# Kernel optimization log

Hardware: AMD Instinct MI355X
Metric: run time of the kernel (lower is better)

Reference implementation:

```python
import math
import jax, jax.numpy as jnp
from jax import lax
import numpy as np

B, SEQ, D_MODEL = 8, 1024, 512
R, K, H = 3, 3, 4
DE, DH, DU, DTR, DCONV, DEMB = 64, 64, 32, 4, 3, 10


def setup_inputs() -> dict:
    key = jax.random.key(0)
    ks = iter(jax.random.split(key, 48))
    def nrm(shape, s=0.05):
        return jax.random.normal(next(ks), shape, jnp.float32) * s
    inp = {}
    inp['x'] = jax.random.normal(next(ks), (B, SEQ, D_MODEL), jnp.float32)
    # Mamba params, leading dims (R, 2) = (layer, fwd/bwd direction)
    inp['m_in_w'] = nrm((R, 2, D_MODEL, 2 * DE))
    inp['m_conv_w'] = nrm((R, 2, DE, DCONV), 0.2)
    inp['m_conv_b'] = nrm((R, 2, DE), 0.1)
    inp['m_xproj_w'] = nrm((R, 2, DE, DTR + 2 * DH))
    inp['m_dt_w'] = nrm((R, 2, DTR, DE), 0.2)
    inp['m_dt_b'] = nrm((R, 2, DE), 0.1)
    inp['m_Alog'] = jnp.broadcast_to(jnp.log(jnp.arange(1, DH + 1, dtype=jnp.float32)), (R, 2, DE, DH)) + jnp.zeros((R, 2, DE, DH), jnp.float32)
    inp['m_D'] = jnp.ones((R, 2, DE), jnp.float32)
    inp['m_out_w'] = nrm((R, 2, DE, D_MODEL))
    # LayerNorm / FFN params per layer
    inp['ln1_g'] = jnp.ones((R, D_MODEL), jnp.float32)
    inp['ln1_b'] = jnp.zeros((R, D_MODEL), jnp.float32)
    inp['ffn_w1'] = nrm((R, D_MODEL, DU))
    inp['ffn_b1'] = jnp.zeros((R, DU), jnp.float32)
    inp['ffn_w2'] = nrm((R, DU, D_MODEL))
    inp['ffn_b2'] = jnp.zeros((R, D_MODEL), jnp.float32)
    inp['ln2_g'] = jnp.ones((R, D_MODEL), jnp.float32)
    inp['ln2_b'] = jnp.zeros((R, D_MODEL), jnp.float32)
    # MAGAC params (N = D_MODEL nodes, in_dim = SEQ)
    inp['psi_emb'] = jax.random.normal(next(ks), (D_MODEL, DEMB), jnp.float32)
    inp['psi'] = jnp.array(1.0, jnp.float32)
    inp['W_q'] = jax.random.normal(next(ks), (DEMB, H, DEMB), jnp.float32)
    inp['W_k'] = jax.random.normal(next(ks), (DEMB, H, DEMB), jnp.float32)
    inp['attn_alpha'] = jnp.array(0.5, jnp.float32)
    inp['F_w'] = nrm((H, DEMB, K + 1, SEQ))
    inp['f_b'] = jax.random.normal(next(ks), (H, DEMB), jnp.float32)
    inp['head_mix'] = jnp.ones((H,), jnp.float32)
    inp['head_w'] = nrm((D_MODEL,))
    inp['head_b'] = jnp.zeros((), jnp.float32)
    return inp


def _layernorm(x, g, b, eps=1e-5):
    mu = x.mean(-1, keepdims=True)
    v = ((x - mu) ** 2).mean(-1, keepdims=True)
    return (x - mu) / jnp.sqrt(v + eps) * g + b


def _mamba(x, in_w, conv_w, conv_b, xproj_w, dt_w, dt_b, Alog, Dp, out_w):
    b, l, _ = x.shape
    xr = x @ in_w                              # (b,l,2*DE)
    xp, res = jnp.split(xr, 2, axis=-1)
    # depthwise causal conv (torch pads k-1 both sides then truncates to l == left-pad k-1)
    xc = xp.transpose(0, 2, 1)                 # (b,DE,l)
    xc = lax.conv_general_dilated(xc, conv_w[:, None, :], (1,), [(DCONV - 1, 0)],
                                  feature_group_count=DE,
                                  dimension_numbers=('NCH', 'OIH', 'NCH'))
    xc = xc + conv_b[None, :, None]
    xp = jax.nn.silu(xc.transpose(0, 2, 1))    # (b,l,DE)
    A = -jnp.exp(Alog)                         # (DE,DH)
    x_dbl = xp @ xproj_w                       # (b,l,DTR+2*DH)
    delta = jax.nn.softplus(x_dbl[..., :DTR] @ dt_w + dt_b)   # (b,l,DE)
    Bm = x_dbl[..., DTR:DTR + DH]
    Cm = x_dbl[..., DTR + DH:]
    dA = jnp.exp(delta[..., None] * A)                         # (b,l,DE,DH)
    dBu = delta[..., None] * Bm[:, :, None, :] * xp[..., None] # (b,l,DE,DH)
    def step(s, inp):
        dAt, dBt, ct = inp
        s = dAt * s + dBt
        return s, jnp.einsum('bdn,bn->bd', s, ct)
    s0 = jnp.zeros((b, DE, DH), x.dtype)
    _, ys = lax.scan(step, s0, (dA.transpose(1, 0, 2, 3), dBu.transpose(1, 0, 2, 3), Cm.transpose(1, 0, 2)))
    y = ys.transpose(1, 0, 2) + xp * Dp
    y = y * jax.nn.sigmoid(res)
    return y @ out_w


def _magac(xg, psi_emb, psi, W_q, W_k, attn_alpha, F_w, f_b, head_mix):
    # xg: (B, N, L); eval-mode deterministic path
    diff = psi_emb[:, None, :] - psi_emb[None, :, :]
    A_base = jax.nn.softmax(jnp.exp(-psi * (diff ** 2).sum(-1)), axis=1)   # (N,N)
    Q = jnp.einsum('nd,dhm->nhm', psi_emb, W_q)
    Kq = jnp.einsum('nd,dhm->nhm', psi_emb, W_k)
    attn = jax.nn.softmax(jnp.einsum('nhd,mhd->hnm', Q, Kq) / math.sqrt(DEMB), axis=-1)
    alpha = jax.nn.sigmoid(attn_alpha)
    A_eff = alpha * A_base[None] + (1.0 - alpha) * attn                    # (H,N,N)
    N = psi_emb.shape[0]
    I = jnp.broadcast_to(jnp.eye(N, dtype=xg.dtype), (H, N, N))
    sup = [I, A_eff]
    for _ in range(K - 1):
        sup.append(2.0 * jnp.matmul(A_eff, sup[-1]) - sup[-2])             # Chebyshev
    sup = jnp.stack(sup, axis=1)                                           # (H,K+1,N,N)
    Wf = jnp.einsum('nd,hdkl->hnkl', psi_emb, F_w)                         # (H,N,K+1,L)
    bf = jnp.einsum('nd,hd->hn', psi_emb, f_b)                             # (H,N)
    x_g = jnp.einsum('hknm,bml->bhknl', sup, xg)                           # (B,H,K+1,N,L)
    out_h = jnp.einsum('bhknl,hnkl->bhn', x_g, Wf) + bf[None]
    mix = jax.nn.softmax(head_mix)
    return jnp.einsum('bhn,h->bn', out_h, mix)


def reference(x, m_in_w, m_conv_w, m_conv_b, m_xproj_w, m_dt_w, m_dt_b, m_Alog, m_D, m_out_w,
              ln1_g, ln1_b, ffn_w1, ffn_b1, ffn_w2, ffn_b2, ln2_g, ln2_b,
              psi_emb, psi, W_q, W_k, attn_alpha, F_w, f_b, head_mix, head_w, head_b):
    for i in range(R):
        mf = (m_in_w[i, 0], m_conv_w[i, 0], m_conv_b[i, 0], m_xproj_w[i, 0], m_dt_w[i, 0],
              m_dt_b[i, 0], m_Alog[i, 0], m_D[i, 0], m_out_w[i, 0])
        mb = (m_in_w[i, 1], m_conv_w[i, 1], m_conv_b[i, 1], m_xproj_w[i, 1], m_dt_w[i, 1],
              m_dt_b[i, 1], m_Alog[i, 1], m_D[i, 1], m_out_w[i, 1])
        y_f = _mamba(x, *mf)
        y_b = jnp.flip(_mamba(jnp.flip(x, 1), *mb), 1)
        y = _layernorm(x + y_f + y_b, ln1_g[i], ln1_b[i])
        z = jax.nn.relu(y @ ffn_w1[i] + ffn_b1[i]) @ ffn_w2[i] + ffn_b2[i]
        x = _layernorm(y + z, ln2_g[i], ln2_b[i])
    g = _magac(x.transpose(0, 2, 1), psi_emb, psi, W_q, W_k, attn_alpha, F_w, f_b, head_mix)
    # eval-mode Bayesian MC: all mc_eval samples identical -> mean=g, var=1e-6
    log_var_node = jnp.full_like(g, jnp.log(jnp.asarray(1e-6, g.dtype)))
    mu = g @ head_w + head_b
    var = jnp.exp(log_var_node) @ (head_w ** 2) + 1e-6
    return mu, jnp.log(var)
```

## Files before the change

### kernel.cpp

```cpp
#include <hip/hip_runtime.h>
#include <math.h>

#define SEQL 1024
#define NB 8
#define DMOD 512

__device__ __forceinline__ float blk_sum4(float v, volatile float* sb) {
#pragma unroll
  for (int off = 32; off; off >>= 1) v += __shfl_xor(v, off, 64);
  int lid = threadIdx.x & 63, wid = threadIdx.x >> 6;
  if (lid == 0) sb[wid] = v;
  __syncthreads();
  float t = sb[0] + sb[1] + sb[2] + sb[3];
  __syncthreads();
  return t;
}
__device__ __forceinline__ float blk_max4(float v, volatile float* sb) {
#pragma unroll
  for (int off = 32; off; off >>= 1) v = fmaxf(v, __shfl_xor(v, off, 64));
  int lid = threadIdx.x & 63, wid = threadIdx.x >> 6;
  if (lid == 0) sb[wid] = v;
  __syncthreads();
  float t = fmaxf(fmaxf(sb[0], sb[1]), fmaxf(sb[2], sb[3]));
  __syncthreads();
  return t;
}

__global__ __launch_bounds__(256) void gemm_f32(
    const float* __restrict__ A, long aStr,
    const float* __restrict__ B, long bStr,
    const float* __restrict__ Dm, long dStr,
    float* __restrict__ C, long cStr, long cChunkStr,
    int M, int N, int K, int lda, int ldb, int ldd, int ldc,
    float alpha, float beta, int kchunks) {
  __shared__ float As[16][68];
  __shared__ float Bs[16][64];
  const int zz = blockIdx.z;
  const int zb = zz / kchunks, kc = zz % kchunks;
  A += (long)zb * aStr + (long)kc * K;
  B += (long)zb * bStr + (long)kc * K * ldb;
  Dm += (long)zb * dStr;
  C += (long)zb * cStr + (long)kc * cChunkStr;
  const int tid = threadIdx.x;
  const int m0 = blockIdx.y * 64, n0 = blockIdx.x * 64;
  const int tx = tid & 15, ty = tid >> 4;
  const int arow = tid >> 2, acol = (tid & 3) << 2;
  const int brow = tid >> 4, bcol = (tid & 15) << 2;
  const bool aOk = (m0 + arow < M);
  const float* Aptr = A + (long)(m0 + arow) * lda + acol;
  const float* Bptr = B + (long)brow * ldb;
  const int bc = n0 + bcol;
  const int kIters = K >> 4;
  float acc[4][4] = {};

  auto loadB = [&](int it) {
    const float* Bk = Bptr + (long)it * 16 * ldb;
    float4 r;
    if (bc + 3 < N) r = *(const float4*)(Bk + bc);
    else {
      r.x = (bc + 0 < N) ? Bk[bc + 0] : 0.f;
      r.y = (bc + 1 < N) ? Bk[bc + 1] : 0.f;
      r.z = (bc + 2 < N) ? Bk[bc + 2] : 0.f;
      r.w = (bc + 3 < N) ? Bk[bc + 3] : 0.f;
    }
    return r;
  };

  float4 av = make_float4(0.f, 0.f, 0.f, 0.f);
  if (aOk) av = *(const float4*)(Aptr);
  float4 bv = loadB(0);

  for (int it = 0; it < kIters; ++it) {
    As[acol + 0][arow] = av.x; As[acol + 1][arow] = av.y;
    As[acol + 2][arow] = av.z; As[acol + 3][arow] = av.w;
    *(float4*)&Bs[brow][bcol] = bv;
    __syncthreads();
    if (it + 1 < kIters) {
      if (aOk) av = *(const float4*)(Aptr + (it + 1) * 16);
      bv = loadB(it + 1);
    }
#pragma unroll
    for (int kk = 0; kk < 16; ++kk) {
      float4 aq = *(const float4*)&As[kk][ty << 2];
      float4 bq = *(const float4*)&Bs[kk][tx << 2];
      float aa[4] = {aq.x, aq.y, aq.z, aq.w};
      float bb[4] = {bq.x, bq.y, bq.z, bq.w};
#pragma unroll
      for (int i = 0; i < 4; ++i)
#pragma unroll
        for (int j = 0; j < 4; ++j) acc[i][j] = fmaf(aa[i], bb[j], acc[i][j]);
    }
    __syncthreads();
  }
#pragma unroll
  for (int i = 0; i < 4; ++i) {
    int row = m0 + (ty << 2) + i;
    if (row >= M) continue;
#pragma unroll
    for (int j = 0; j < 4; ++j) {
      int col = n0 + (tx << 2) + j;
      if (col >= N) continue;
      float v = alpha * acc[i][j];
      if (beta != 0.f) v += beta * Dm[(long)row * ldd + col];
      C[(long)row * ldc + col] = v;
    }
  }
}

__global__ __launch_bounds__(256) void conv_silu(
    const float* __restrict__ xr, float* __restrict__ xp,
    const float* __restrict__ cw, const float* __restrict__ cb) {
  int dir = blockIdx.y;
  int idx = blockIdx.x * 256 + threadIdx.x;
  const float* xrp = xr + (long)dir * 1048576;
  float* xpp = xp + (long)dir * 524288;
  const float* w = cw + dir * 192;
  int e = idx & 63;
  int t = (idx >> 6) & 1023;
  long rb = (long)(idx >> 6) * 128;
  float w0 = w[e * 3 + 0], w1 = w[e * 3 + 1], w2 = w[e * 3 + 2];
  float acc = cb[dir * 64 + e] + w2 * xrp[rb + e];
  if (dir == 0) {
    if (t >= 1) acc += w1 * xrp[rb - 128 + e];
    if (t >= 2) acc += w0 * xrp[rb - 256 + e];
  } else {
    if (t <= 1022) acc += w1 * xrp[rb + 128 + e];
    if (t <= 1021) acc += w0 * xrp[rb + 256 + e];
  }
  xpp[idx] = acc / (1.f + __expf(-acc));
}

__global__ __launch_bounds__(64) void proj_kernel(
    const float* __restrict__ xp, const float* __restrict__ pw,
    const float* __restrict__ dw, const float* __restrict__ db,
    float* __restrict__ dl, float* __restrict__ Bm, float* __restrict__ Cm) {
  int tok = blockIdx.x, dir = blockIdx.y, j = threadIdx.x;
  const float* xpp = xp + (long)dir * 524288 + (long)tok * 64;
  const float* w = pw + dir * 8448;
  __shared__ float xs[64];
  __shared__ float dpre[4];
  xs[j] = xpp[j];
  __syncthreads();
  float aB = 0.f, aC = 0.f, aD = 0.f;
  for (int k = 0; k < 64; ++k) {
    float xv = xs[k];
    const float* wr = w + k * 132;
    aB = fmaf(xv, wr[4 + j], aB);
    aC = fmaf(xv, wr[68 + j], aC);
    aD = fmaf(xv, wr[j & 3], aD);
  }
  long ob = (long)dir * 524288 + (long)tok * 64;
  Bm[ob + j] = aB;
  Cm[ob + j] = aC;
  if (j < 4) dpre[j] = aD;
  __syncthreads();
  const float* dwp = dw + dir * 256;
  float dv = db[dir * 64 + j];
#pragma unroll
  for (int r = 0; r < 4; ++r) dv = fmaf(dpre[r], dwp[r * 64 + j], dv);
  dl[ob + j] = fmaxf(dv, 0.f) + log1pf(__expf(-fabsf(dv)));
}

__global__ __launch_bounds__(64) void scan_p1(
    const float* __restrict__ dl, const float* __restrict__ Bm,
    const float* __restrict__ xp, const float* __restrict__ Alog,
    float* __restrict__ Aprod, float* __restrict__ Send) {
  int d = blockIdx.x, b = blockIdx.y;
  int dir = blockIdx.z >> 4, c = blockIdx.z & 15;
  int n = threadIdx.x;
  long doff = (long)dir * 524288;
  int tln = c * 64 + n;
  int tgn = dir ? 1023 - tln : tln;
  float dlv_v = dl[doff + ((long)b * 1024 + tgn) * 64 + d];
  float xpv_v = xp[doff + ((long)b * 1024 + tgn) * 64 + d];
  float a_dn = -__expf(Alog[dir * 4096 + d * 64 + n]);
  const float* Bp = Bm + doff + (long)b * 65536;
  float s = 0.f, ap = 1.f;
#pragma unroll 8
  for (int st = 0; st < 64; ++st) {
    float dlv = __shfl(dlv_v, st);
    float xpv = __shfl(xpv_v, st);
    int tl = c * 64 + st;
    int tg = dir ? 1023 - tl : tl;
    float bt = Bp[(long)tg * 64 + n];
    float a = __expf(dlv * a_dn);
    ap *= a;
    s = fmaf(a, s, (dlv * xpv) * bt);
  }
  long sidx = ((long)((dir * 8 + b) * 64 + d)) * 1024 + c * 64 + n;
  Aprod[sidx] = ap;
  Send[sidx] = s;
}

__global__ __launch_bounds__(64) void scan_p2(
    const float* __restrict__ Aprod, const float* __restrict__ Send,
    float* __restrict__ Sin) {
  int d = blockIdx.x, b = blockIdx.y, dir = blockIdx.z;
  int n = threadIdx.x;
  long base = ((long)((dir * 8 + b) * 64 + d)) * 1024;
  float s = 0.f;
#pragma unroll
  for (int c = 0; c < 16; ++c) {
    Sin[base + c * 64 + n] = s;
    s = fmaf(Aprod[base + c * 64 + n], s, Send[base + c * 64 + n]);
  }
}

__global__ __launch_bounds__(64) void scan_p3(
    const float* __restrict__ dl, const float* __restrict__ Bm,
    const float* __restrict__ Cm, const float* __restrict__ xp,
    const float* __restrict__ xr, const float* __restrict__ Alog,
    const float* __restrict__ Dp, const float* __restrict__ Sin,
    float* __restrict__ ycat) {
  __shared__ float sP[16 * 65];
  int d = blockIdx.x, b = blockIdx.y;
  int dir = blockIdx.z >> 4, c = blockIdx.z & 15;
  int n = threadIdx.x;
  long doff = (long)dir * 524288;
  int tln = c * 64 + n;
  int tgn = dir ? 1023 - tln : tln;
  float dlv_v = dl[doff + ((long)b * 1024 + tgn) * 64 + d];
  float xpv_v = xp[doff + ((long)b * 1024 + tgn) * 64 + d];
  float a_dn = -__expf(Alog[dir * 4096 + d * 64 + n]);
  float dpd = Dp[dir * 64 + d];
  const float* Bp = Bm + doff + (long)b * 65536;
  const float* Cp = Cm + doff + (long)b * 65536;
  const float* xrp = xr + (long)dir * 1048576 + (long)b * 131072;
  long sidx = ((long)((dir * 8 + b) * 64 + d)) * 1024 + c * 64 + n;
  float s = Sin[sidx];
  int r4 = n >> 2, q4 = n & 3;
  for (int sb = 0; sb < 4; ++sb) {
#pragma unroll
    for (int k = 0; k < 16; ++k) {
      int st = sb * 16 + k;
      float dlv = __shfl(dlv_v, st);
      float xpv = __shfl(xpv_v, st);
      int tl = c * 64 + st;
      int tg = dir ? 1023 - tl : tl;
      float bt = Bp[(long)tg * 64 + n];
      float ct = Cp[(long)tg * 64 + n];
      float a = __expf(dlv * a_dn);
      s = fmaf(a, s, (dlv * xpv) * bt);
      sP[k * 65 + n] = s * ct;
    }
    __syncthreads();
    float p = 0.f;
#pragma unroll
    for (int k = 0; k < 16; ++k) p += sP[r4 * 65 + q4 * 16 + k];
    p += __shfl_xor(p, 1, 64);
    p += __shfl_xor(p, 2, 64);
    float xpv_r = __shfl(xpv_v, sb * 16 + r4);
    if (q4 == 0) {
      int tl = c * 64 + sb * 16 + r4;
      int tg = dir ? 1023 - tl : tl;
      float rres = xrp[(long)tg * 128 + 64 + d];
      ycat[((long)b * 1024 + tg) * 128 + dir * 64 + d] =
          (p + xpv_r * dpd) * (1.f / (1.f + __expf(-rres)));
    }
    __syncthreads();
  }
}

__global__ __launch_bounds__(256) void ln_ffn_ln(
    float* __restrict__ x, const float* __restrict__ g1, const float* __restrict__ b1v,
    const float* __restrict__ w1, const float* __restrict__ bb1,
    const float* __restrict__ w2, const float* __restrict__ bb2,
    const float* __restrict__ g2, const float* __restrict__ b2v) {
  __shared__ float ybuf[512];
  __shared__ float rbuf[256];
  __shared__ float zbuf[32];
  __shared__ float red[4];
  int tok = blockIdx.x, tid = threadIdx.x;
  float* row = x + (long)tok * 512;
  float v0 = row[tid], v1 = row[tid + 256];
  float mu = blk_sum4(v0 + v1, red) * (1.f / 512.f);
  float d0 = v0 - mu, d1 = v1 - mu;
  float var = blk_sum4(d0 * d0 + d1 * d1, red) * (1.f / 512.f);
  float rstd = 1.f / sqrtf(var + 1e-5f);
  float y0 = d0 * rstd * g1[tid] + b1v[tid];
  float y1 = d1 * rstd * g1[tid + 256] + b1v[tid + 256];
  ybuf[tid] = y0; ybuf[tid + 256] = y1;
  __syncthreads();
  int u = tid & 31, seg = tid >> 5;
  float p = 0.f;
  int k0 = seg * 64;
#pragma unroll 8
  for (int k = 0; k < 64; ++k) p = fmaf(ybuf[k0 + k], w1[(k0 + k) * 32 + u], p);
  rbuf[seg * 32 + u] = p;
  __syncthreads();
  if (tid < 32) {
    float zv = bb1[tid];
#pragma unroll
    for (int sg = 0; sg < 8; ++sg) zv += rbuf[sg * 32 + tid];
    zbuf[tid] = fmaxf(zv, 0.f);
  }
  __syncthreads();
  float h0 = y0 + bb2[tid];
  float h1 = y1 + bb2[tid + 256];
#pragma unroll
  for (int uu = 0; uu < 32; ++uu) {
    float zv = zbuf[uu];
    h0 = fmaf(zv, w2[uu * 512 + tid], h0);
    h1 = fmaf(zv, w2[uu * 512 + tid + 256], h1);
  }
  float mu2 = blk_sum4(h0 + h1, red) * (1.f / 512.f);
  float e0 = h0 - mu2, e1 = h1 - mu2;
  float var2 = blk_sum4(e0 * e0 + e1 * e1, red) * (1.f / 512.f);
  float rstd2 = 1.f / sqrtf(var2 + 1e-5f);
  row[tid] = e0 * rstd2 * g2[tid] + b2v[tid];
  row[tid + 256] = e1 * rstd2 * g2[tid + 256] + b2v[tid + 256];
}

__global__ __launch_bounds__(64) void qk_kernel(
    const float* __restrict__ e, const float* __restrict__ Wq,
    const float* __restrict__ Wk, float* __restrict__ Qb, float* __restrict__ Kb) {
  int n = blockIdx.x, j = threadIdx.x;
  __shared__ float en[10];
  if (j < 10) en[j] = e[n * 10 + j];
  __syncthreads();
  if (j < 40) {
    float q = 0.f, k = 0.f;
#pragma unroll
    for (int dd = 0; dd < 10; ++dd) {
      q = fmaf(en[dd], Wq[dd * 40 + j], q);
      k = fmaf(en[dd], Wk[dd * 40 + j], k);
    }
    Qb[n * 40 + j] = q;
    Kb[n * 40 + j] = k;
  }
}

__global__ __launch_bounds__(256) void aeff_kernel(
    const float* __restrict__ e, const float* __restrict__ Qb,
    const float* __restrict__ Kb, const float* __restrict__ psi_p,
    const float* __restrict__ alpha_p, float* __restrict__ Aef) {
  int n = blockIdx.x, h = blockIdx.y, tid = threadIdx.x;
  __shared__ float s_at[512];
  __shared__ float s_bs[512];
  __shared__ float qn[10];
  __shared__ float en[10];
  __shared__ float red[4];
  if (tid < 10) { qn[tid] = Qb[n * 40 + h * 10 + tid]; en[tid] = e[n * 10 + tid]; }
  __syncthreads();
  float psi = psi_p[0];
  float alpha = 1.f / (1.f + __expf(-alpha_p[0]));
  const float isq = 0.3162277660168379f;
  for (int m = tid; m < 512; m += 256) {
    float sc = 0.f, d2 = 0.f;
#pragma unroll
    for (int dd = 0; dd < 10; ++dd) {
      sc = fmaf(qn[dd], Kb[m * 40 + h * 10 + dd], sc);
      float df = en[dd] - e[m * 10 + dd];
      d2 = fmaf(df, df, d2);
    }
    s_at[m] = sc * isq;
    s_bs[m] = __expf(-psi * d2);
  }
  __syncthreads();
  float m1 = -1e30f, m2 = -1e30f;
  for (int m = tid; m < 512; m += 256) { m1 = fmaxf(m1, s_at[m]); m2 = fmaxf(m2, s_bs[m]); }
  m1 = blk_max4(m1, red);
  m2 = blk_max4(m2, red);
  float e1 = 0.f, e2 = 0.f;
  for (int m = tid; m < 512; m += 256) {
    float a = __expf(s_at[m] - m1); s_at[m] = a; e1 += a;
    float bq = __expf(s_bs[m] - m2); s_bs[m] = bq; e2 += bq;
  }
  e1 = blk_sum4(e1, red);
  e2 = blk_sum4(e2, red);
  float r1 = (1.f - alpha) / e1, r2 = alpha / e2;
  float* outp = Aef + (long)h * 262144 + (long)n * 512;
  for (int m = tid; m < 512; m += 256) outp[m] = r2 * s_bs[m] + r1 * s_at[m];
}

__global__ void xpose_kernel(const float* __restrict__ DbufP,
                             float* __restrict__ X3, float* __restrict__ X2s,
                             float* __restrict__ X13, float* __restrict__ X02) {
  int idx = blockIdx.x * 256 + threadIdx.x;
  if (idx >= 163840) return;
  int c = idx % 80;
  int m = (idx / 80) % 512;
  int h = idx / 40960;
  int d = c >> 3, b = c & 7;
  long base = (long)(b * 160 + h * 40 + d * 4) * 512 + m;
  float k0 = 0.f, k1 = 0.f, k2 = 0.f, k3 = 0.f;
#pragma unroll
  for (int p = 0; p < 4; ++p) {
    const float* Dp_ = DbufP + (long)p * 655360;
    k0 += Dp_[base];
    k1 += Dp_[base + 512];
    k2 += Dp_[base + 1024];
    k3 += Dp_[base + 1536];
  }
  X3[idx] = k3;
  X2s[idx] = k2;
  X13[idx] = k1 - 3.f * k3;
  X02[idx] = k0 - k2;
}

__global__ void outh_kernel(const float* __restrict__ e, const float* __restrict__ fb,
                            const float* __restrict__ Zt, const float* __restrict__ hm,
                            float* __restrict__ g) {
  int idx = blockIdx.x * 256 + threadIdx.x;
  if (idx >= 4096) return;
  int n = idx & 511, b = idx >> 9;
  float h0 = hm[0], h1 = hm[1], h2 = hm[2], h3 = hm[3];
  float mx = fmaxf(fmaxf(h0, h1), fmaxf(h2, h3));
  float x0 = __expf(h0 - mx), x1 = __expf(h1 - mx), x2 = __expf(h2 - mx), x3 = __expf(h3 - mx);
  float es = x0 + x1 + x2 + x3;
  float mixv[4] = {x0 / es, x1 / es, x2 / es, x3 / es};
  float acc = 0.f;
  for (int h = 0; h < 4; ++h) {
    float oh = 0.f;
#pragma unroll
    for (int dd = 0; dd < 10; ++dd) {
      float ev = e[n * 10 + dd];
      float v = Zt[((long)h * 512 + n) * 80 + dd * 8 + b] + fb[h * 10 + dd];
      oh = fmaf(ev, v, oh);
    }
    acc = fmaf(mixv[h], oh, acc);
  }
  g[b * 512 + n] = acc;
}

__global__ __launch_bounds__(256) void head_kernel(
    const float* __restrict__ g, const float* __restrict__ hw,
    const float* __restrict__ hb, float* __restrict__ out) {
  __shared__ float red[4];
  int b = blockIdx.x, tid = threadIdx.x;
  float w0 = hw[tid], w1 = hw[tid + 256];
  float v = g[b * 512 + tid] * w0 + g[b * 512 + tid + 256] * w1;
  float q = w0 * w0 + w1 * w1;
  float mu = blk_sum4(v, red);
  float s2 = blk_sum4(q, red);
  if (tid == 0) {
    out[b] = mu + hb[0];
    out[8 + b] = logf(1e-6f * s2 + 1e-6f);
  }
}

extern "C" void kernel_launch(void* const* d_in, const int* in_sizes, int n_in,
                              void* d_out, int out_size, void* d_ws, size_t ws_size,
                              hipStream_t stream) {
  (void)in_sizes; (void)n_in; (void)out_size; (void)ws_size;
  const float* x0    = (const float*)d_in[0];
  const float* in_w  = (const float*)d_in[1];
  const float* cw    = (const float*)d_in[2];
  const float* cb    = (const float*)d_in[3];
  const float* pw    = (const float*)d_in[4];
  const float* dtw   = (const float*)d_in[5];
  const float* dtb   = (const float*)d_in[6];
  const float* Alog  = (const float*)d_in[7];
  const float* Dpar  = (const float*)d_in[8];
  const float* ow    = (const float*)d_in[9];
  const float* l1g   = (const float*)d_in[10];
  const float* l1b   = (const float*)d_in[11];
  const float* fw1   = (const float*)d_in[12];
  const float* fb1   = (const float*)d_in[13];
  const float* fw2   = (const float*)d_in[14];
  const float* fb2   = (const float*)d_in[15];
  const float* l2g   = (const float*)d_in[16];
  const float* l2b   = (const float*)d_in[17];
  const float* emb   = (const float*)d_in[18];
  const float* psi   = (const float*)d_in[19];
  const float* Wq    = (const float*)d_in[20];
  const float* Wk    = (const float*)d_in[21];
  const float* aal   = (const float*)d_in[22];
  const float* Fw    = (const float*)d_in[23];
  const float* fbv   = (const float*)d_in[24];
  const float* hmix  = (const float*)d_in[25];
  const float* hw    = (const float*)d_in[26];
  const float* hb    = (const float*)d_in[27];
  float* out = (float*)d_out;

  float* ws = (float*)d_ws;
  float* xA   = ws;
  float* xB   = xA + 4194304;
  float* scr  = xB + 4194304;
  float* xr   = scr;
  float* xp   = xr + 2097152;
  float* dl   = xp + 1048576;
  float* Bm   = dl + 1048576;
  float* Cm   = Bm + 1048576;
  float* ycat = Cm + 1048576;
  float* Aprod = scr + 7340032;
  float* Send  = Aprod + 1048576;
  float* Sin   = Send + 1048576;
  float* Qb    = scr;
  float* Kb    = Qb + 20480;
  float* Aef   = Kb + 20480;
  float* DbufP = Aef + 1048576;
  float* X3    = DbufP + 2621440;
  float* X2s   = X3 + 163840;
  float* X13   = X2s + 163840;
  float* X02   = X13 + 163840;
  float* Z2    = X02 + 163840;
  float* Z1    = Z2 + 163840;
  float* Zt    = Z1 + 163840;
  float* gb    = Zt + 163840;

  const float* xin = x0;
  float* bufs[3] = {xA, xB, xA};
  for (int i = 0; i < 3; ++i) {
    float* xout = bufs[i];
    gemm_f32<<<dim3(2, 128, 2), 256, 0, stream>>>(
        xin, 0, in_w + (long)i * 131072, 65536, xin, 0, xr, 1048576, 0,
        8192, 128, 512, 512, 128, 0, 128, 1.f, 0.f, 1);
    conv_silu<<<dim3(2048, 2), 256, 0, stream>>>(xr, xp, cw + i * 384, cb + i * 128);
    proj_kernel<<<dim3(8192, 2), 64, 0, stream>>>(
        xp, pw + i * 16896, dtw + i * 512, dtb + i * 128, dl, Bm, Cm);
    scan_p1<<<dim3(64, 8, 32), 64, 0, stream>>>(
        dl, Bm, xp, Alog + i * 8192, Aprod, Send);
    scan_p2<<<dim3(64, 8, 2), 64, 0, stream>>>(Aprod, Send, Sin);
    scan_p3<<<dim3(64, 8, 32), 64, 0, stream>>>(
        dl, Bm, Cm, xp, xr, Alog + i * 8192, Dpar + i * 128, Sin, ycat);
    gemm_f32<<<dim3(8, 128, 1), 256, 0, stream>>>(
        ycat, 0, ow + (long)i * 65536, 0, xin, 0, xout, 0, 0,
        8192, 512, 128, 128, 512, 512, 512, 1.f, 1.f, 1);
    ln_ffn_ln<<<8192, 256, 0, stream>>>(
        xout, l1g + i * 512, l1b + i * 512, fw1 + i * 16384, fb1 + i * 32,
        fw2 + i * 16384, fb2 + i * 512, l2g + i * 512, l2b + i * 512);
    xin = xout;
  }
  qk_kernel<<<512, 64, 0, stream>>>(emb, Wq, Wk, Qb, Kb);
  aeff_kernel<<<dim3(512, 4), 256, 0, stream>>>(emb, Qb, Kb, psi, aal, Aef);
  gemm_f32<<<dim3(8, 3, 32), 256, 0, stream>>>(
      Fw, 0, xA, 524288, Fw, 0, DbufP, 81920, 655360,
      160, 512, 256, 1024, 512, 0, 512, 1.f, 0.f, 4);
  xpose_kernel<<<640, 256, 0, stream>>>(DbufP, X3, X2s, X13, X02);
  gemm_f32<<<dim3(2, 8, 4), 256, 0, stream>>>(
      Aef, 262144, X3, 40960, X2s, 40960, Z2, 40960, 0,
      512, 80, 512, 512, 80, 80, 80, 4.f, 2.f, 1);
  gemm_f32<<<dim3(2, 8, 4), 256, 0, stream>>>(
      Aef, 262144, Z2, 40960, X13, 40960, Z1, 40960, 0,
      512, 80, 512, 512, 80, 80, 80, 1.f, 1.f, 1);
  gemm_f32<<<dim3(2, 8, 4), 256, 0, stream>>>(
      Aef, 262144, Z1, 40960, X02, 40960, Zt, 40960, 0,
      512, 80, 512, 512, 80, 80, 80, 1.f, 1.f, 1);
  outh_kernel<<<16, 256, 0, stream>>>(emb, fbv, Zt, hmix, gb);
  head_kernel<<<8, 256, 0, stream>>>(gb, hw, hb, out);
}
```

Before: 825.9 us.

## Double-buffer GEMM shared tiles and process two tokens per LN-FFN block

The GEMM kernel now uses ping-pong shared-memory buffers for its A and B tiles. This drops one barrier per k-iteration and lets the store of the next tile follow the compute on the current one. The fused LayerNorm-FFN-LayerNorm kernel now handles two tokens per block, reusing each w1/w2 weight load across both tokens. It also computes mean and variance in a single pass (sum and sum of squares), which removes two of the block reductions. The single-pass variance is slightly less numerically robust, and the doubled shared memory may lower occupancy.

```diff
diff --git a/kernel.cpp b/kernel.cpp
--- a/kernel.cpp
+++ b/kernel.cpp
@@ -33,8 +33,8 @@
     float* __restrict__ C, long cStr, long cChunkStr,
     int M, int N, int K, int lda, int ldb, int ldd, int ldc,
     float alpha, float beta, int kchunks) {
-  __shared__ float As[16][68];
-  __shared__ float Bs[16][64];
+  __shared__ float As[2][16][68];
+  __shared__ float Bs[2][16][64];
   const int zz = blockIdx.z;
   const int zb = zz / kchunks, kc = zz % kchunks;
   A += (long)zb * aStr + (long)kc * K;
@@ -69,20 +69,22 @@
   float4 av = make_float4(0.f, 0.f, 0.f, 0.f);
   if (aOk) av = *(const float4*)(Aptr);
   float4 bv = loadB(0);
+  As[0][acol + 0][arow] = av.x; As[0][acol + 1][arow] = av.y;
+  As[0][acol + 2][arow] = av.z; As[0][acol + 3][arow] = av.w;
+  *(float4*)&Bs[0][brow][bcol] = bv;
 
   for (int it = 0; it < kIters; ++it) {
-    As[acol + 0][arow] = av.x; As[acol + 1][arow] = av.y;
-    As[acol + 2][arow] = av.z; As[acol + 3][arow] = av.w;
-    *(float4*)&Bs[brow][bcol] = bv;
+    const int cur = it & 1;
     __syncthreads();
-    if (it + 1 < kIters) {
+    const bool more = (it + 1 < kIters);
+    if (more) {
       if (aOk) av = *(const float4*)(Aptr + (it + 1) * 16);
       bv = loadB(it + 1);
     }
 #pragma unroll
     for (int kk = 0; kk < 16; ++kk) {
-      float4 aq = *(const float4*)&As[kk][ty << 2];
-      float4 bq = *(const float4*)&Bs[kk][tx << 2];
+      float4 aq = *(const float4*)&As[cur][kk][ty << 2];
+      float4 bq = *(const float4*)&Bs[cur][kk][tx << 2];
       float aa[4] = {aq.x, aq.y, aq.z, aq.w};
       float bb[4] = {bq.x, bq.y, bq.z, bq.w};
 #pragma unroll
@@ -90,7 +92,12 @@
 #pragma unroll
         for (int j = 0; j < 4; ++j) acc[i][j] = fmaf(aa[i], bb[j], acc[i][j]);
     }
-    __syncthreads();
+    if (more) {
+      const int nxt = cur ^ 1;
+      As[nxt][acol + 0][arow] = av.x; As[nxt][acol + 1][arow] = av.y;
+      As[nxt][acol + 2][arow] = av.z; As[nxt][acol + 3][arow] = av.w;
+      *(float4*)&Bs[nxt][brow][bcol] = bv;
+    }
   }
 #pragma unroll
   for (int i = 0; i < 4; ++i) {
@@ -266,49 +273,105 @@
     const float* __restrict__ w1, const float* __restrict__ bb1,
     const float* __restrict__ w2, const float* __restrict__ bb2,
     const float* __restrict__ g2, const float* __restrict__ b2v) {
-  __shared__ float ybuf[512];
-  __shared__ float rbuf[256];
-  __shared__ float zbuf[32];
-  __shared__ float red[4];
-  int tok = blockIdx.x, tid = threadIdx.x;
-  float* row = x + (long)tok * 512;
-  float v0 = row[tid], v1 = row[tid + 256];
-  float mu = blk_sum4(v0 + v1, red) * (1.f / 512.f);
-  float d0 = v0 - mu, d1 = v1 - mu;
-  float var = blk_sum4(d0 * d0 + d1 * d1, red) * (1.f / 512.f);
-  float rstd = 1.f / sqrtf(var + 1e-5f);
-  float y0 = d0 * rstd * g1[tid] + b1v[tid];
-  float y1 = d1 * rstd * g1[tid + 256] + b1v[tid + 256];
-  ybuf[tid] = y0; ybuf[tid + 256] = y1;
+  __shared__ float ybuf[2][512];
+  __shared__ float rbuf[2][256];
+  __shared__ float zbuf[2][32];
+  __shared__ float red4[16];
+  int tid = threadIdx.x;
+  int lid = tid & 63, wid = tid >> 6;
+  float* row0 = x + (long)blockIdx.x * 1024;
+  float* row1 = row0 + 512;
+  float a0 = row0[tid], b0 = row0[tid + 256];
+  float a1 = row1[tid], b1 = row1[tid + 256];
+  float s0 = a0 + b0, q0 = a0 * a0 + b0 * b0;
+  float s1 = a1 + b1, q1 = a1 * a1 + b1 * b1;
+#pragma unroll
+  for (int off = 32; off; off >>= 1) {
+    s0 += __shfl_xor(s0, off, 64); q0 += __shfl_xor(q0, off, 64);
+    s1 += __shfl_xor(s1, off, 64); q1 += __shfl_xor(q1, off, 64);
+  }
+  if (lid == 0) {
+    red4[wid * 4 + 0] = s0; red4[wid * 4 + 1] = q0;
+    red4[wid * 4 + 2] = s1; red4[wid * 4 + 3] = q1;
+  }
+  __syncthreads();
+  float S0 = red4[0] + red4[4] + red4[8] + red4[12];
+  float Q0 = red4[1] + red4[5] + red4[9] + red4[13];
+  float S1 = red4[2] + red4[6] + red4[10] + red4[14];
+  float Q1 = red4[3] + red4[7] + red4[11] + red4[15];
+  float mu0 = S0 * (1.f / 512.f), mu1 = S1 * (1.f / 512.f);
+  float r0 = 1.f / sqrtf(Q0 * (1.f / 512.f) - mu0 * mu0 + 1e-5f);
+  float r1 = 1.f / sqrtf(Q1 * (1.f / 512.f) - mu1 * mu1 + 1e-5f);
+  float g1a = g1[tid], g1b = g1[tid + 256];
+  float b1a = b1v[tid], b1b = b1v[tid + 256];
+  float y0a = (a0 - mu0) * r0 * g1a + b1a;
+  float y0b = (b0 - mu0) * r0 * g1b + b1b;
+  float y1a = (a1 - mu1) * r1 * g1a + b1a;
+  float y1b = (b1 - mu1) * r1 * g1b + b1b;
+  ybuf[0][tid] = y0a; ybuf[0][tid + 256] = y0b;
+  ybuf[1][tid] = y1a; ybuf[1][tid + 256] = y1b;
   __syncthreads();
   int u = tid & 31, seg = tid >> 5;
-  float p = 0.f;
   int k0 = seg * 64;
-#pragma unroll 8
-  for (int k = 0; k < 64; ++k) p = fmaf(ybuf[k0 + k], w1[(k0 + k) * 32 + u], p);
-  rbuf[seg * 32 + u] = p;
-  __syncthreads();
-  if (tid < 32) {
-    float zv = bb1[tid];
-#pragma unroll
-    for (int sg = 0; sg < 8; ++sg) zv += rbuf[sg * 32 + tid];
-    zbuf[tid] = fmaxf(zv, 0.f);
-  }
-  __syncthreads();
-  float h0 = y0 + bb2[tid];
-  float h1 = y1 + bb2[tid + 256];
+  float p0 = 0.f, p1 = 0.f;
+#pragma unroll
+  for (int k = 0; k < 64; k += 4) {
+    float4 ya = *(const float4*)&ybuf[0][k0 + k];
+    float4 yb = *(const float4*)&ybuf[1][k0 + k];
+    float w1v0 = w1[(k0 + k + 0) * 32 + u];
+    float w1v1 = w1[(k0 + k + 1) * 32 + u];
+    float w1v2 = w1[(k0 + k + 2) * 32 + u];
+    float w1v3 = w1[(k0 + k + 3) * 32 + u];
+    p0 = fmaf(ya.w, w1v3, fmaf(ya.z, w1v2, fmaf(ya.y, w1v1, fmaf(ya.x, w1v0, p0))));
+    p1 = fmaf(yb.w, w1v3, fmaf(yb.z, w1v2, fmaf(yb.y, w1v1, fmaf(yb.x, w1v0, p1))));
+  }
+  rbuf[0][seg * 32 + u] = p0;
+  rbuf[1][seg * 32 + u] = p1;
+  __syncthreads();
+  if (tid < 64) {
+    int t = tid >> 5, uu = tid & 31;
+    float zv = bb1[uu];
+#pragma unroll
+    for (int sg = 0; sg < 8; ++sg) zv += rbuf[t][sg * 32 + uu];
+    zbuf[t][uu] = fmaxf(zv, 0.f);
+  }
+  __syncthreads();
+  float bb2a = bb2[tid], bb2b = bb2[tid + 256];
+  float h0a = y0a + bb2a, h0b = y0b + bb2b;
+  float h1a = y1a + bb2a, h1b = y1b + bb2b;
 #pragma unroll
   for (int uu = 0; uu < 32; ++uu) {
-    float zv = zbuf[uu];
-    h0 = fmaf(zv, w2[uu * 512 + tid], h0);
-    h1 = fmaf(zv, w2[uu * 512 + tid + 256], h1);
-  }
-  float mu2 = blk_sum4(h0 + h1, red) * (1.f / 512.f);
-  float e0 = h0 - mu2, e1 = h1 - mu2;
-  float var2 = blk_sum4(e0 * e0 + e1 * e1, red) * (1.f / 512.f);
-  float rstd2 = 1.f / sqrtf(var2 + 1e-5f);
-  row[tid] = e0 * rstd2 * g2[tid] + b2v[tid];
-  row[tid + 256] = e1 * rstd2 * g2[tid + 256] + b2v[tid + 256];
+    float wa = w2[uu * 512 + tid], wb = w2[uu * 512 + tid + 256];
+    float z0 = zbuf[0][uu], z1 = zbuf[1][uu];
+    h0a = fmaf(z0, wa, h0a); h1a = fmaf(z1, wa, h1a);
+    h0b = fmaf(z0, wb, h0b); h1b = fmaf(z1, wb, h1b);
+  }
+  s0 = h0a + h0b; q0 = h0a * h0a + h0b * h0b;
+  s1 = h1a + h1b; q1 = h1a * h1a + h1b * h1b;
+#pragma unroll
+  for (int off = 32; off; off >>= 1) {
+    s0 += __shfl_xor(s0, off, 64); q0 += __shfl_xor(q0, off, 64);
+    s1 += __shfl_xor(s1, off, 64); q1 += __shfl_xor(q1, off, 64);
+  }
+  __syncthreads();
+  if (lid == 0) {
+    red4[wid * 4 + 0] = s0; red4[wid * 4 + 1] = q0;
+    red4[wid * 4 + 2] = s1; red4[wid * 4 + 3] = q1;
+  }
+  __syncthreads();
+  S0 = red4[0] + red4[4] + red4[8] + red4[12];
+  Q0 = red4[1] + red4[5] + red4[9] + red4[13];
+  S1 = red4[2] + red4[6] + red4[10] + red4[14];
+  Q1 = red4[3] + red4[7] + red4[11] + red4[15];
+  mu0 = S0 * (1.f / 512.f); mu1 = S1 * (1.f / 512.f);
+  r0 = 1.f / sqrtf(Q0 * (1.f / 512.f) - mu0 * mu0 + 1e-5f);
+  r1 = 1.f / sqrtf(Q1 * (1.f / 512.f) - mu1 * mu1 + 1e-5f);
+  float g2a = g2[tid], g2b = g2[tid + 256];
+  float b2a = b2v[tid], b2b = b2v[tid + 256];
+  row0[tid] = (h0a - mu0) * r0 * g2a + b2a;
+  row0[tid + 256] = (h0b - mu0) * r0 * g2b + b2b;
+  row1[tid] = (h1a - mu1) * r1 * g2a + b2a;
+  row1[tid + 256] = (h1b - mu1) * r1 * g2b + b2b;
 }
 
 __global__ __launch_bounds__(64) void qk_kernel(
@@ -517,7 +580,7 @@
     gemm_f32<<<dim3(8, 128, 1), 256, 0, stream>>>(
         ycat, 0, ow + (long)i * 65536, 0, xin, 0, xout, 0, 0,
         8192, 512, 128, 128, 512, 512, 512, 1.f, 1.f, 1);
-    ln_ffn_ln<<<8192, 256, 0, stream>>>(
+    ln_ffn_ln<<<4096, 256, 0, stream>>>(
         xout, l1g + i * 512, l1b + i * 512, fw1 + i * 16384, fb1 + i * 32,
         fw2 + i * 16384, fb2 + i * 512, l2g + i * 512, l2b + i * 512);
     xin = xout;
```

After: 771.7 us. 1.07x faster.
